# Performance work log

Hardware: AMD Instinct MI355X
Metric: run time of the kernel (lower is better)

The kernel has to match this reference:

```python
import jax, jax.numpy as jnp
import numpy as np

N_NODES = 100000
N_EDGES = 6400000
F_IN, F_HID, F_OUT = 5, 5, 10


def setup_inputs() -> dict:
    key = jax.random.key(0)
    ks = jax.random.split(key, 9)
    x = jax.random.normal(ks[0], (N_NODES, F_IN), dtype=jnp.float32)
    src = jax.random.randint(ks[1], (N_EDGES,), 0, N_NODES, dtype=jnp.int32)
    dst = jax.random.randint(ks[2], (N_EDGES,), 0, N_NODES, dtype=jnp.int32)
    s1 = 1.0 / np.sqrt(F_IN)
    s2 = 1.0 / np.sqrt(F_HID)
    W_self1 = jax.random.uniform(ks[3], (F_IN, F_HID), jnp.float32, -s1, s1)
    W_neigh1 = jax.random.uniform(ks[4], (F_IN, F_HID), jnp.float32, -s1, s1)
    b1 = jnp.zeros((F_HID,), jnp.float32)
    W_self2 = jax.random.uniform(ks[5], (F_HID, F_OUT), jnp.float32, -s2, s2)
    W_neigh2 = jax.random.uniform(ks[6], (F_HID, F_OUT), jnp.float32, -s2, s2)
    b2 = jnp.zeros((F_OUT,), jnp.float32)
    return {"x": x, "src": src, "dst": dst,
            "W_self1": W_self1, "W_neigh1": W_neigh1, "b1": b1,
            "W_self2": W_self2, "W_neigh2": W_neigh2, "b2": b2}


def _sage_mean(h, src, dst, W_self, W_neigh, b):
    # DGL SAGEConv (mean): out = h @ W_self + mean_{u->v}(h_u) @ W_neigh + b
    msg = h[src]                                        # [E, F] gather
    agg = jax.ops.segment_sum(msg, dst, num_segments=N_NODES)   # [N, F]
    deg = jax.ops.segment_sum(jnp.ones((src.shape[0],), h.dtype), dst,
                              num_segments=N_NODES)     # [N]
    h_neigh = agg / jnp.maximum(deg, 1.0)[:, None]
    return h @ W_self + h_neigh @ W_neigh + b


def reference(x, src, dst, W_self1, W_neigh1, b1, W_self2, W_neigh2, b2):
    h = jax.nn.sigmoid(_sage_mean(x, src, dst, W_self1, W_neigh1, b1))
    out = jax.nn.sigmoid(_sage_mean(h, src, dst, W_self2, W_neigh2, b2))
    return out
```

## Files before the change

kernel.cpp:

```cpp
#include <hip/hip_runtime.h>
#include <hip/hip_fp16.h>
#include <math.h>


#define F_IN  5
#define F_HID 5
#define F_OUT 10

#define NBSHIFT 7
#define NPB     (1 << NBSHIFT)
#define PBLK    1024
#define CHUNK   8192
#define EPT     8
#define BSTRIDE 9216
#define SBLK    512
#define SPT     18
#define LPN2    8
#define LBLK    256

__device__ __forceinline__ float sigmoidf(float v) {
    return 1.0f / (1.0f + __expf(-v));
}

__global__ void prep(const float* __restrict__ x, uint4* __restrict__ xh,
                     int* __restrict__ bcursor, int N, int NB) {
    int v = blockIdx.x * blockDim.x + threadIdx.x;
    if (v < NB) bcursor[v] = v * BSTRIDE;
    if (v >= N) return;
    const float* xr = x + (size_t)v * 5;
    float4 a = *(const float4*)xr;
    float a4 = xr[4];
    unsigned short h0 = __half_as_ushort(__float2half_rn(a.x));
    unsigned short h1 = __half_as_ushort(__float2half_rn(a.y));
    unsigned short h2 = __half_as_ushort(__float2half_rn(a.z));
    unsigned short h3 = __half_as_ushort(__float2half_rn(a.w));
    unsigned short h4 = __half_as_ushort(__float2half_rn(a4));
    uint4 o;
    o.x = (unsigned)h0 | ((unsigned)h1 << 16);
    o.y = (unsigned)h2 | ((unsigned)h3 << 16);
    o.z = (unsigned)h4;
    o.w = 0;
    xh[v] = o;
}

__global__ void partition(const int* __restrict__ src, const int* __restrict__ dst,
                          int* __restrict__ bcursor, int* __restrict__ packed,
                          int E, int NB) {
    __shared__ int cnt[PBLK], excl[PBLK], adj[PBLK];
    __shared__ int wsum[16];
    __shared__ int buf[CHUNK];
    __shared__ unsigned char dlow[CHUNK];
    int t = threadIdx.x;
    int lane = t & 63, w = t >> 6;
    cnt[t] = 0;
    __syncthreads();
    int base = blockIdx.x * CHUNK;
    int end  = min(base + CHUNK, E);
    int esd[EPT];
    int ebp[EPT];
    #pragma unroll
    for (int j = 0; j < EPT; ++j) {
        int i = base + t + j * PBLK;
        if (i < end) {
            int sv = src[i], d = dst[i];
            int b  = d >> NBSHIFT;
            int p  = atomicAdd(&cnt[b], 1);
            esd[j] = sv | ((d & (NPB - 1)) << 17);
            ebp[j] = (b << 14) | p;
        }
    }
    __syncthreads();
    int v = cnt[t];
    int incl = v;
    #pragma unroll
    for (int off = 1; off < 64; off <<= 1) {
        int u = __shfl_up(incl, off, 64);
        if (lane >= off) incl += u;
    }
    if (lane == 63) wsum[w] = incl;
    __syncthreads();
    if (t < 16) {
        int s = wsum[t];
        #pragma unroll
        for (int off = 1; off < 16; off <<= 1) {
            int u = __shfl_up(s, off, 16);
            if (t >= off) s += u;
        }
        wsum[t] = s;
    }
    __syncthreads();
    int wbase = (w > 0) ? wsum[w - 1] : 0;
    excl[t] = incl - v + wbase;
    __syncthreads();
    if (t < NB) {
        int cb = cnt[t];
        int go = cb ? atomicAdd(&bcursor[t], cb) : 0;
        adj[t] = go - excl[t];
    }
    __syncthreads();
    #pragma unroll
    for (int j = 0; j < EPT; ++j) {
        int i = base + t + j * PBLK;
        if (i < end) {
            int b   = ebp[j] >> 14;
            int pos = excl[b] + (ebp[j] & 0x3FFF);
            buf[pos]  = (esd[j] & 0x1FFFF) | (b << 17);
            dlow[pos] = (unsigned char)(esd[j] >> 17);
        }
    }
    __syncthreads();
    int cval = end - base;
    for (int p = t; p < cval; p += PBLK) {
        int e = buf[p];
        int b = e >> 17;
        packed[adj[b] + p] = (e & 0x1FFFF) | ((int)dlow[p] << 17);
    }
}

__global__ void __launch_bounds__(SBLK, 8)
sortagg1(const uint4* __restrict__ xh, int* __restrict__ packed,
         const int* __restrict__ bcursor,
         const float* __restrict__ Ws, const float* __restrict__ Wn,
         const float* __restrict__ bias,
         uint4* __restrict__ hp, int* __restrict__ starts,
         int* __restrict__ degs, int N) {
    __shared__ int buf[BSTRIDE];
    __shared__ int ncnt[NPB], nst[NPB];
    __shared__ int w0sum;
    int b = blockIdx.x, t = threadIdx.x;
    int s0  = b * BSTRIDE;
    int cnt = min(bcursor[b] - s0, BSTRIDE);
    if (t < NPB) ncnt[t] = 0;
    __syncthreads();
    int myv[SPT];
    short myp[SPT];
    #pragma unroll
    for (int j = 0; j < SPT; ++j) {
        int i = t + j * SBLK;
        if (i < cnt) {
            int e = packed[s0 + i];
            myv[j] = e;
            myp[j] = (short)atomicAdd(&ncnt[(e >> 17) & (NPB - 1)], 1);
        }
    }
    __syncthreads();
    if (t < NPB) {
        int lane = t & 63;
        int v = ncnt[t];
        int incl = v;
        #pragma unroll
        for (int off = 1; off < 64; off <<= 1) {
            int u = __shfl_up(incl, off, 64);
            if (lane >= off) incl += u;
        }
        if (t == 63) w0sum = incl;
        nst[t] = incl - v;
    }
    __syncthreads();
    if (t >= 64 && t < NPB) nst[t] += w0sum;
    __syncthreads();
    if (t < NPB) {
        int node = (b << NBSHIFT) + t;
        if (node < N) { starts[node] = s0 + nst[t]; degs[node] = ncnt[t]; }
    }
    __syncthreads();
    #pragma unroll
    for (int j = 0; j < SPT; ++j) {
        int i = t + j * SBLK;
        if (i < cnt) {
            int e = myv[j];
            buf[nst[(e >> 17) & (NPB - 1)] + (int)myp[j]] = e;
        }
    }
    __syncthreads();
    for (int i = t; i < cnt; i += SBLK)
        packed[s0 + i] = buf[i] & 0x1FFFF;
    int sub = t & 3, ln = t >> 2;
    int node = (b << NBSHIFT) + ln;
    float a0 = 0, a1 = 0, a2 = 0, a3 = 0, a4 = 0;
    int dg = 0;
    if (node < N) {
        int st = nst[ln];
        dg = ncnt[ln];
        for (int k = sub; k < dg; k += 4) {
            int u = buf[st + k] & 0x1FFFF;
            uint4 q = xh[u];
            float2 f01 = __half22float2(*(const __half2*)&q.x);
            float2 f23 = __half22float2(*(const __half2*)&q.y);
            float2 f45 = __half22float2(*(const __half2*)&q.z);
            a0 += f01.x; a1 += f01.y; a2 += f23.x; a3 += f23.y; a4 += f45.x;
        }
    }
    #pragma unroll
    for (int off = 2; off > 0; off >>= 1) {
        a0 += __shfl_down(a0, off, 4);
        a1 += __shfl_down(a1, off, 4);
        a2 += __shfl_down(a2, off, 4);
        a3 += __shfl_down(a3, off, 4);
        a4 += __shfl_down(a4, off, 4);
    }
    if (sub != 0 || node >= N) return;
    float rd = 1.0f / fmaxf((float)dg, 1.0f);
    float ni[F_IN] = { a0 * rd, a1 * rd, a2 * rd, a3 * rd, a4 * rd };
    uint4 qs = xh[node];
    float2 s01 = __half22float2(*(const __half2*)&qs.x);
    float2 s23 = __half22float2(*(const __half2*)&qs.y);
    float2 s45 = __half22float2(*(const __half2*)&qs.z);
    float xi[F_IN] = { s01.x, s01.y, s23.x, s23.y, s45.x };
    unsigned short hu[6];
    #pragma unroll
    for (int j = 0; j < F_HID; ++j) {
        float acc = bias[j];
        #pragma unroll
        for (int f = 0; f < F_IN; ++f)
            acc += xi[f] * Ws[f * F_HID + j] + ni[f] * Wn[f * F_HID + j];
        hu[j] = __half_as_ushort(__float2half_rn(sigmoidf(acc)));
    }
    hu[5] = 0;
    uint4 o;
    o.x = (unsigned)hu[0] | ((unsigned)hu[1] << 16);
    o.y = (unsigned)hu[2] | ((unsigned)hu[3] << 16);
    o.z = (unsigned)hu[4];
    o.w = 0;
    hp[node] = o;
}

__global__ void layer2(const uint4* __restrict__ hp, const int* __restrict__ eidx,
                       const int* __restrict__ starts, const int* __restrict__ degs,
                       const float* __restrict__ Ws, const float* __restrict__ Wn,
                       const float* __restrict__ b,
                       float* __restrict__ out, int N) {
    int tid = blockIdx.x * blockDim.x + threadIdx.x;
    int v   = tid >> 3;
    int sub = threadIdx.x & (LPN2 - 1);
    if (v >= N) return;
    int st = starts[v], dg = degs[v];
    float s0 = 0, s1 = 0, s2 = 0, s3 = 0, s4 = 0;
    for (int k = sub; k < dg; k += LPN2) {
        int u = eidx[st + k];
        uint4 q = hp[u];
        float2 f01 = __half22float2(*(const __half2*)&q.x);
        float2 f23 = __half22float2(*(const __half2*)&q.y);
        float2 f45 = __half22float2(*(const __half2*)&q.z);
        s0 += f01.x; s1 += f01.y; s2 += f23.x; s3 += f23.y; s4 += f45.x;
    }
    #pragma unroll
    for (int off = LPN2 / 2; off > 0; off >>= 1) {
        s0 += __shfl_down(s0, off, LPN2);
        s1 += __shfl_down(s1, off, LPN2);
        s2 += __shfl_down(s2, off, LPN2);
        s3 += __shfl_down(s3, off, LPN2);
        s4 += __shfl_down(s4, off, LPN2);
    }
    if (sub != 0) return;
    float rd = 1.0f / fmaxf((float)dg, 1.0f);
    float ni[F_HID] = { s0 * rd, s1 * rd, s2 * rd, s3 * rd, s4 * rd };
    uint4 q = hp[v];
    float2 f01 = __half22float2(*(const __half2*)&q.x);
    float2 f23 = __half22float2(*(const __half2*)&q.y);
    float2 f45 = __half22float2(*(const __half2*)&q.z);
    float hi[F_HID] = { f01.x, f01.y, f23.x, f23.y, f45.x };
    #pragma unroll
    for (int j = 0; j < F_OUT; ++j) {
        float acc = b[j];
        #pragma unroll
        for (int f = 0; f < F_HID; ++f)
            acc += hi[f] * Ws[f * F_OUT + j] + ni[f] * Wn[f * F_OUT + j];
        out[(size_t)v * F_OUT + j] = sigmoidf(acc);
    }
}

extern "C" void kernel_launch(void* const* d_in, const int* in_sizes, int n_in,
                              void* d_out, int out_size, void* d_ws, size_t ws_size,
                              hipStream_t stream) {
    const float* x   = (const float*)d_in[0];
    const int*   src = (const int*)d_in[1];
    const int*   dst = (const int*)d_in[2];
    const float* Ws1 = (const float*)d_in[3];
    const float* Wn1 = (const float*)d_in[4];
    const float* b1  = (const float*)d_in[5];
    const float* Ws2 = (const float*)d_in[6];
    const float* Wn2 = (const float*)d_in[7];
    const float* b2  = (const float*)d_in[8];
    float* out = (float*)d_out;

    const int N  = in_sizes[0] / F_IN;
    const int E  = in_sizes[1];
    const int NB = (N + NPB - 1) >> NBSHIFT;

    int*   bcursor = (int*)d_ws;
    uint4* xh      = (uint4*)(bcursor + 1024);
    int*   starts  = (int*)(xh + N);
    int*   degs    = starts + N;
    int*   packed  = degs + N;
    uint4* hp      = (uint4*)(packed + (size_t)NB * BSTRIDE);

    const int ablocks = (E + CHUNK - 1) / CHUNK;
    const int pgrid   = (N + 255) / 256;
    const int lgrid   = ((size_t)N * LPN2 + LBLK - 1) / LBLK;

    prep<<<pgrid, 256, 0, stream>>>(x, xh, bcursor, N, NB);
    partition<<<ablocks, PBLK, 0, stream>>>(src, dst, bcursor, packed, E, NB);
    sortagg1<<<NB, SBLK, 0, stream>>>(xh, packed, bcursor, Ws1, Wn1, b1,
                                      hp, starts, degs, N);
    layer2<<<lgrid, LBLK, 0, stream>>>(hp, packed, starts, degs, Ws2, Wn2, b2, out, N);
}
```

Before: 209.7 us.

## Fuse layer-2 into sort kernel via grid barrier; fold prep into partition

Folds the fp16 conversion of x into the partition kernel and replaces the bucket-cursor init with a memset. Merges the layer-1 and layer-2 kernels into one persistent kernel. Each block keeps its sorted neighbour list in shared memory and waits at a global atomic barrier until all hp values are written, then computes layer 2 directly. This drops the starts/degs/packed write-back and re-read plus one kernel launch. It relies on all NB (~782) blocks being co-resident, since otherwise the spin barrier could deadlock.

```diff
diff --git a/kernel.cpp b/kernel.cpp
--- a/kernel.cpp
+++ b/kernel.cpp
@@ -15,43 +15,37 @@
 #define BSTRIDE 9216
 #define SBLK    512
 #define SPT     18
-#define LPN2    8
-#define LBLK    256
 
 __device__ __forceinline__ float sigmoidf(float v) {
     return 1.0f / (1.0f + __expf(-v));
 }
 
-__global__ void prep(const float* __restrict__ x, uint4* __restrict__ xh,
-                     int* __restrict__ bcursor, int N, int NB) {
-    int v = blockIdx.x * blockDim.x + threadIdx.x;
-    if (v < NB) bcursor[v] = v * BSTRIDE;
-    if (v >= N) return;
-    const float* xr = x + (size_t)v * 5;
-    float4 a = *(const float4*)xr;
-    float a4 = xr[4];
-    unsigned short h0 = __half_as_ushort(__float2half_rn(a.x));
-    unsigned short h1 = __half_as_ushort(__float2half_rn(a.y));
-    unsigned short h2 = __half_as_ushort(__float2half_rn(a.z));
-    unsigned short h3 = __half_as_ushort(__float2half_rn(a.w));
-    unsigned short h4 = __half_as_ushort(__float2half_rn(a4));
-    uint4 o;
-    o.x = (unsigned)h0 | ((unsigned)h1 << 16);
-    o.y = (unsigned)h2 | ((unsigned)h3 << 16);
-    o.z = (unsigned)h4;
-    o.w = 0;
-    xh[v] = o;
-}
-
-__global__ void partition(const int* __restrict__ src, const int* __restrict__ dst,
+__global__ void partition(const float* __restrict__ x,
+                          const int* __restrict__ src, const int* __restrict__ dst,
                           int* __restrict__ bcursor, int* __restrict__ packed,
-                          int E, int NB) {
+                          uint4* __restrict__ xh, int E, int N, int NB) {
     __shared__ int cnt[PBLK], excl[PBLK], adj[PBLK];
     __shared__ int wsum[16];
     __shared__ int buf[CHUNK];
     __shared__ unsigned char dlow[CHUNK];
     int t = threadIdx.x;
     int lane = t & 63, w = t >> 6;
+    if (t < NPB) {
+        int v = (blockIdx.x << NBSHIFT) + t;
+        if (v < N) {
+            const float* xr = x + (size_t)v * 5;
+            float4 a = *(const float4*)xr;
+            float a4 = xr[4];
+            uint4 o;
+            o.x = (unsigned)__half_as_ushort(__float2half_rn(a.x)) |
+                  ((unsigned)__half_as_ushort(__float2half_rn(a.y)) << 16);
+            o.y = (unsigned)__half_as_ushort(__float2half_rn(a.z)) |
+                  ((unsigned)__half_as_ushort(__float2half_rn(a.w)) << 16);
+            o.z = (unsigned)__half_as_ushort(__float2half_rn(a4));
+            o.w = 0;
+            xh[v] = o;
+        }
+    }
     cnt[t] = 0;
     __syncthreads();
     int base = blockIdx.x * CHUNK;
@@ -95,7 +89,7 @@
     if (t < NB) {
         int cb = cnt[t];
         int go = cb ? atomicAdd(&bcursor[t], cb) : 0;
-        adj[t] = go - excl[t];
+        adj[t] = t * BSTRIDE + go - excl[t];
     }
     __syncthreads();
     #pragma unroll
@@ -118,18 +112,20 @@
 }
 
 __global__ void __launch_bounds__(SBLK, 8)
-sortagg1(const uint4* __restrict__ xh, int* __restrict__ packed,
-         const int* __restrict__ bcursor,
-         const float* __restrict__ Ws, const float* __restrict__ Wn,
-         const float* __restrict__ bias,
-         uint4* __restrict__ hp, int* __restrict__ starts,
-         int* __restrict__ degs, int N) {
+fused12(const uint4* __restrict__ xh, const int* __restrict__ packed,
+        const int* __restrict__ bcursor,
+        const float* __restrict__ Ws1, const float* __restrict__ Wn1,
+        const float* __restrict__ b1,
+        const float* __restrict__ Ws2, const float* __restrict__ Wn2,
+        const float* __restrict__ b2,
+        uint4* __restrict__ hp, float* __restrict__ out,
+        int* __restrict__ done, int N, int NB) {
     __shared__ int buf[BSTRIDE];
     __shared__ int ncnt[NPB], nst[NPB];
     __shared__ int w0sum;
     int b = blockIdx.x, t = threadIdx.x;
     int s0  = b * BSTRIDE;
-    int cnt = min(bcursor[b] - s0, BSTRIDE);
+    int cnt = min(bcursor[b], BSTRIDE);
     if (t < NPB) ncnt[t] = 0;
     __syncthreads();
     int myv[SPT];
@@ -159,11 +155,6 @@
     __syncthreads();
     if (t >= 64 && t < NPB) nst[t] += w0sum;
     __syncthreads();
-    if (t < NPB) {
-        int node = (b << NBSHIFT) + t;
-        if (node < N) { starts[node] = s0 + nst[t]; degs[node] = ncnt[t]; }
-    }
-    __syncthreads();
     #pragma unroll
     for (int j = 0; j < SPT; ++j) {
         int i = t + j * SBLK;
@@ -173,100 +164,100 @@
         }
     }
     __syncthreads();
-    for (int i = t; i < cnt; i += SBLK)
-        packed[s0 + i] = buf[i] & 0x1FFFF;
     int sub = t & 3, ln = t >> 2;
     int node = (b << NBSHIFT) + ln;
-    float a0 = 0, a1 = 0, a2 = 0, a3 = 0, a4 = 0;
-    int dg = 0;
-    if (node < N) {
-        int st = nst[ln];
-        dg = ncnt[ln];
-        for (int k = sub; k < dg; k += 4) {
-            int u = buf[st + k] & 0x1FFFF;
-            uint4 q = xh[u];
+    int st = nst[ln], dg = ncnt[ln];
+    {
+        float a0 = 0, a1 = 0, a2 = 0, a3 = 0, a4 = 0;
+        if (node < N) {
+            for (int k = sub; k < dg; k += 4) {
+                int u = buf[st + k] & 0x1FFFF;
+                uint4 q = xh[u];
+                float2 f01 = __half22float2(*(const __half2*)&q.x);
+                float2 f23 = __half22float2(*(const __half2*)&q.y);
+                float2 f45 = __half22float2(*(const __half2*)&q.z);
+                a0 += f01.x; a1 += f01.y; a2 += f23.x; a3 += f23.y; a4 += f45.x;
+            }
+        }
+        #pragma unroll
+        for (int off = 2; off > 0; off >>= 1) {
+            a0 += __shfl_down(a0, off, 4);
+            a1 += __shfl_down(a1, off, 4);
+            a2 += __shfl_down(a2, off, 4);
+            a3 += __shfl_down(a3, off, 4);
+            a4 += __shfl_down(a4, off, 4);
+        }
+        if (sub == 0 && node < N) {
+            float rd = 1.0f / fmaxf((float)dg, 1.0f);
+            float ni[F_IN] = { a0 * rd, a1 * rd, a2 * rd, a3 * rd, a4 * rd };
+            uint4 qs = xh[node];
+            float2 s01 = __half22float2(*(const __half2*)&qs.x);
+            float2 s23 = __half22float2(*(const __half2*)&qs.y);
+            float2 s45 = __half22float2(*(const __half2*)&qs.z);
+            float xi[F_IN] = { s01.x, s01.y, s23.x, s23.y, s45.x };
+            unsigned short hu[5];
+            #pragma unroll
+            for (int j = 0; j < F_HID; ++j) {
+                float acc = b1[j];
+                #pragma unroll
+                for (int f = 0; f < F_IN; ++f)
+                    acc += xi[f] * Ws1[f * F_HID + j] + ni[f] * Wn1[f * F_HID + j];
+                hu[j] = __half_as_ushort(__float2half_rn(sigmoidf(acc)));
+            }
+            uint4 o;
+            o.x = (unsigned)hu[0] | ((unsigned)hu[1] << 16);
+            o.y = (unsigned)hu[2] | ((unsigned)hu[3] << 16);
+            o.z = (unsigned)hu[4];
+            o.w = 0;
+            hp[node] = o;
+        }
+    }
+    __syncthreads();
+    if (t == 0) {
+        __threadfence();
+        __hip_atomic_fetch_add(done, 1, __ATOMIC_RELAXED, __HIP_MEMORY_SCOPE_AGENT);
+        while (__hip_atomic_load(done, __ATOMIC_RELAXED, __HIP_MEMORY_SCOPE_AGENT) < NB)
+            __builtin_amdgcn_s_sleep(2);
+    }
+    __syncthreads();
+    __threadfence();
+    {
+        float c0 = 0, c1 = 0, c2 = 0, c3 = 0, c4 = 0;
+        if (node < N) {
+            for (int k = sub; k < dg; k += 4) {
+                int u = buf[st + k] & 0x1FFFF;
+                uint4 q = hp[u];
+                float2 f01 = __half22float2(*(const __half2*)&q.x);
+                float2 f23 = __half22float2(*(const __half2*)&q.y);
+                float2 f45 = __half22float2(*(const __half2*)&q.z);
+                c0 += f01.x; c1 += f01.y; c2 += f23.x; c3 += f23.y; c4 += f45.x;
+            }
+        }
+        #pragma unroll
+        for (int off = 2; off > 0; off >>= 1) {
+            c0 += __shfl_down(c0, off, 4);
+            c1 += __shfl_down(c1, off, 4);
+            c2 += __shfl_down(c2, off, 4);
+            c3 += __shfl_down(c3, off, 4);
+            c4 += __shfl_down(c4, off, 4);
+        }
+        if (sub == 0 && node < N) {
+            float rd = 1.0f / fmaxf((float)dg, 1.0f);
+            float ni[F_HID] = { c0 * rd, c1 * rd, c2 * rd, c3 * rd, c4 * rd };
+            uint4 q = hp[node];
             float2 f01 = __half22float2(*(const __half2*)&q.x);
             float2 f23 = __half22float2(*(const __half2*)&q.y);
             float2 f45 = __half22float2(*(const __half2*)&q.z);
-            a0 += f01.x; a1 += f01.y; a2 += f23.x; a3 += f23.y; a4 += f45.x;
-        }
-    }
-    #pragma unroll
-    for (int off = 2; off > 0; off >>= 1) {
-        a0 += __shfl_down(a0, off, 4);
-        a1 += __shfl_down(a1, off, 4);
-        a2 += __shfl_down(a2, off, 4);
-        a3 += __shfl_down(a3, off, 4);
-        a4 += __shfl_down(a4, off, 4);
-    }
-    if (sub != 0 || node >= N) return;
-    float rd = 1.0f / fmaxf((float)dg, 1.0f);
-    float ni[F_IN] = { a0 * rd, a1 * rd, a2 * rd, a3 * rd, a4 * rd };
-    uint4 qs = xh[node];
-    float2 s01 = __half22float2(*(const __half2*)&qs.x);
-    float2 s23 = __half22float2(*(const __half2*)&qs.y);
-    float2 s45 = __half22float2(*(const __half2*)&qs.z);
-    float xi[F_IN] = { s01.x, s01.y, s23.x, s23.y, s45.x };
-    unsigned short hu[6];
-    #pragma unroll
-    for (int j = 0; j < F_HID; ++j) {
-        float acc = bias[j];
-        #pragma unroll
-        for (int f = 0; f < F_IN; ++f)
-            acc += xi[f] * Ws[f * F_HID + j] + ni[f] * Wn[f * F_HID + j];
-        hu[j] = __half_as_ushort(__float2half_rn(sigmoidf(acc)));
-    }
-    hu[5] = 0;
-    uint4 o;
-    o.x = (unsigned)hu[0] | ((unsigned)hu[1] << 16);
-    o.y = (unsigned)hu[2] | ((unsigned)hu[3] << 16);
-    o.z = (unsigned)hu[4];
-    o.w = 0;
-    hp[node] = o;
-}
-
-__global__ void layer2(const uint4* __restrict__ hp, const int* __restrict__ eidx,
-                       const int* __restrict__ starts, const int* __restrict__ degs,
-                       const float* __restrict__ Ws, const float* __restrict__ Wn,
-                       const float* __restrict__ b,
-                       float* __restrict__ out, int N) {
-    int tid = blockIdx.x * blockDim.x + threadIdx.x;
-    int v   = tid >> 3;
-    int sub = threadIdx.x & (LPN2 - 1);
-    if (v >= N) return;
-    int st = starts[v], dg = degs[v];
-    float s0 = 0, s1 = 0, s2 = 0, s3 = 0, s4 = 0;
-    for (int k = sub; k < dg; k += LPN2) {
-        int u = eidx[st + k];
-        uint4 q = hp[u];
-        float2 f01 = __half22float2(*(const __half2*)&q.x);
-        float2 f23 = __half22float2(*(const __half2*)&q.y);
-        float2 f45 = __half22float2(*(const __half2*)&q.z);
-        s0 += f01.x; s1 += f01.y; s2 += f23.x; s3 += f23.y; s4 += f45.x;
-    }
-    #pragma unroll
-    for (int off = LPN2 / 2; off > 0; off >>= 1) {
-        s0 += __shfl_down(s0, off, LPN2);
-        s1 += __shfl_down(s1, off, LPN2);
-        s2 += __shfl_down(s2, off, LPN2);
-        s3 += __shfl_down(s3, off, LPN2);
-        s4 += __shfl_down(s4, off, LPN2);
-    }
-    if (sub != 0) return;
-    float rd = 1.0f / fmaxf((float)dg, 1.0f);
-    float ni[F_HID] = { s0 * rd, s1 * rd, s2 * rd, s3 * rd, s4 * rd };
-    uint4 q = hp[v];
-    float2 f01 = __half22float2(*(const __half2*)&q.x);
-    float2 f23 = __half22float2(*(const __half2*)&q.y);
-    float2 f45 = __half22float2(*(const __half2*)&q.z);
-    float hi[F_HID] = { f01.x, f01.y, f23.x, f23.y, f45.x };
-    #pragma unroll
-    for (int j = 0; j < F_OUT; ++j) {
-        float acc = b[j];
-        #pragma unroll
-        for (int f = 0; f < F_HID; ++f)
-            acc += hi[f] * Ws[f * F_OUT + j] + ni[f] * Wn[f * F_OUT + j];
-        out[(size_t)v * F_OUT + j] = sigmoidf(acc);
+            float hi[F_HID] = { f01.x, f01.y, f23.x, f23.y, f45.x };
+            #pragma unroll
+            for (int j = 0; j < F_OUT; ++j) {
+                float acc = b2[j];
+                #pragma unroll
+                for (int f = 0; f < F_HID; ++f)
+                    acc += hi[f] * Ws2[f * F_OUT + j] + ni[f] * Wn2[f * F_OUT + j];
+                out[(size_t)node * F_OUT + j] = sigmoidf(acc);
+            }
+        }
     }
 }
 
@@ -288,20 +279,17 @@
     const int E  = in_sizes[1];
     const int NB = (N + NPB - 1) >> NBSHIFT;
 
-    int*   bcursor = (int*)d_ws;
-    uint4* xh      = (uint4*)(bcursor + 1024);
-    int*   starts  = (int*)(xh + N);
-    int*   degs    = starts + N;
-    int*   packed  = degs + N;
+    int*   ctrl    = (int*)d_ws;
+    int*   bcursor = ctrl;
+    int*   done    = ctrl + 1023;
+    uint4* xh      = (uint4*)(ctrl + 1024);
+    int*   packed  = (int*)(xh + N);
     uint4* hp      = (uint4*)(packed + (size_t)NB * BSTRIDE);
 
     const int ablocks = (E + CHUNK - 1) / CHUNK;
-    const int pgrid   = (N + 255) / 256;
-    const int lgrid   = ((size_t)N * LPN2 + LBLK - 1) / LBLK;
-
-    prep<<<pgrid, 256, 0, stream>>>(x, xh, bcursor, N, NB);
-    partition<<<ablocks, PBLK, 0, stream>>>(src, dst, bcursor, packed, E, NB);
-    sortagg1<<<NB, SBLK, 0, stream>>>(xh, packed, bcursor, Ws1, Wn1, b1,
-                                      hp, starts, degs, N);
-    layer2<<<lgrid, LBLK, 0, stream>>>(hp, packed, starts, degs, Ws2, Wn2, b2, out, N);
-}
+
+    (void)hipMemsetAsync(ctrl, 0, 1024 * sizeof(int), stream);
+    partition<<<ablocks, PBLK, 0, stream>>>(x, src, dst, bcursor, packed, xh, E, N, NB);
+    fused12<<<NB, SBLK, 0, stream>>>(xh, packed, bcursor, Ws1, Wn1, b1,
+                                     Ws2, Wn2, b2, hp, out, done, N, NB);
+}
```

After: 378.2 us. 80.4% more time.
